# Performance work log

Measured on AMD Instinct MI355X. Metric: run time of the kernel, lower is better.

Reference implementation:

```python
import jax, jax.numpy as jnp
import numpy as np

# FP4 E2M1 representable magnitudes (sign handled separately)
_FP4_GRID = np.array([0.0, 0.5, 1.0, 1.5, 2.0, 3.0, 4.0, 6.0], dtype=np.float32)
_FP4_MIDS = (_FP4_GRID[:-1] + _FP4_GRID[1:]) / 2.0  # round-to-nearest boundaries


def fp4_quant_dequant(w):
    """Per-tensor absmax-scaled round-to-nearest FP4 (E2M1) fake quantization."""
    grid = jnp.asarray(_FP4_GRID, dtype=w.dtype)
    mids = jnp.asarray(_FP4_MIDS, dtype=w.dtype)
    scale = jnp.max(jnp.abs(w)) / 6.0  # map absmax -> top FP4 level
    a = jnp.abs(w) / scale
    idx = jnp.searchsorted(mids, a)  # nearest grid index via boundary search
    return grid[idx] * jnp.sign(w) * scale


def fp4_linear(x, W, b):
    # dequantized-weight matmul + bias, as in FP4Linear
    Wq = fp4_quant_dequant(W)
    return x @ Wq.T + b


def setup_inputs() -> dict:
    key = jax.random.key(0)
    k1, k2, k3, k4, k5 = jax.random.split(key, 5)
    B, D_IN, D_H, D_OUT = 8192, 2048, 8192, 2048
    x = jax.random.normal(k1, (B, D_IN), dtype=jnp.float32)
    W1 = jax.random.normal(k2, (D_H, D_IN), dtype=jnp.float32) * 0.02
    b1 = jax.random.normal(k3, (D_H,), dtype=jnp.float32) * 0.02
    W2 = jax.random.normal(k4, (D_OUT, D_H), dtype=jnp.float32) * 0.02
    b2 = jax.random.normal(k5, (D_OUT,), dtype=jnp.float32) * 0.02
    return {"x": x, "W1": W1, "b1": b1, "W2": W2, "b2": b2}


def reference(x, W1, b1, W2, b2):
    h = jax.nn.relu(fp4_linear(x, W1, b1))  # [B, hidden]
    y = fp4_linear(h, W2, b2)                # [B, out]
    return y
```

## Files before the change

kernel.cpp:

```cpp
#include <hip/hip_runtime.h>
#include <hip/hip_bf16.h>
#include <stdint.h>

typedef __attribute__((ext_vector_type(8))) short short8;
typedef __attribute__((ext_vector_type(4))) float f32x4;

#define AS1 __attribute__((address_space(1)))
#define AS3 __attribute__((address_space(3)))

static __device__ __forceinline__ unsigned short f2bf(float f) {
    unsigned int u = __float_as_uint(f);
    u += 0x7FFFu + ((u >> 16) & 1u);
    return (unsigned short)(u >> 16);
}

__global__ void init_amax(unsigned int* amax) {
    if (threadIdx.x < 2) amax[threadIdx.x] = 0u;
}

__global__ void absmax_kernel(const float4* __restrict__ w, size_t n4,
                              unsigned int* __restrict__ out) {
    float m = 0.0f;
    size_t i = (size_t)blockIdx.x * blockDim.x + threadIdx.x;
    size_t stride = (size_t)gridDim.x * blockDim.x;
    for (; i < n4; i += stride) {
        float4 v = w[i];
        m = fmaxf(m, fmaxf(fmaxf(fabsf(v.x), fabsf(v.y)),
                           fmaxf(fabsf(v.z), fabsf(v.w))));
    }
    #pragma unroll
    for (int off = 32; off > 0; off >>= 1)
        m = fmaxf(m, __shfl_down(m, off, 64));
    __shared__ float sm[4];
    int lane = threadIdx.x & 63, wid = threadIdx.x >> 6;
    if (lane == 0) sm[wid] = m;
    __syncthreads();
    if (threadIdx.x == 0) {
        float bm = fmaxf(fmaxf(sm[0], sm[1]), fmaxf(sm[2], sm[3]));
        atomicMax(out, __float_as_uint(bm));
    }
}

static __device__ __forceinline__ unsigned short quant_one(float wv, float scale) {
    float a = fabsf(wv) / scale;
    int idx = (a > 0.25f) + (a > 0.75f) + (a > 1.25f) + (a > 1.75f)
            + (a > 2.5f)  + (a > 3.5f)  + (a > 5.0f);
    const unsigned long long lo = 0x3FC03F803F000000ull;
    const unsigned long long hi = 0x40C0408040404000ull;
    unsigned long long tab = (idx < 4) ? lo : hi;
    unsigned short mag = (unsigned short)(tab >> ((idx & 3) * 16));
    unsigned short sgn = (unsigned short)((__float_as_uint(wv) >> 16) & 0x8000u);
    return (unsigned short)(mag | sgn);
}

__global__ void quant_kernel(const float4* __restrict__ w, size_t n4,
                             const unsigned int* __restrict__ amax,
                             ushort4* __restrict__ q) {
    const float scale = __uint_as_float(*amax) / 6.0f;
    size_t i = (size_t)blockIdx.x * blockDim.x + threadIdx.x;
    size_t stride = (size_t)gridDim.x * blockDim.x;
    for (; i < n4; i += stride) {
        float4 v = w[i];
        ushort4 o;
        o.x = quant_one(v.x, scale);
        o.y = quant_one(v.y, scale);
        o.z = quant_one(v.z, scale);
        o.w = quant_one(v.w, scale);
        q[i] = o;
    }
}

__global__ void cast_bf16_kernel(const float4* __restrict__ x, size_t n4,
                                 ushort4* __restrict__ o) {
    size_t i = (size_t)blockIdx.x * blockDim.x + threadIdx.x;
    size_t stride = (size_t)gridDim.x * blockDim.x;
    for (; i < n4; i += stride) {
        float4 v = x[i];
        ushort4 r;
        r.x = f2bf(v.x); r.y = f2bf(v.y); r.z = f2bf(v.z); r.w = f2bf(v.w);
        o[i] = r;
    }
}


#define STG(gp, ldsoff)                                                         \
    do {                                                                        \
        __builtin_amdgcn_global_load_lds((const AS1 unsigned int*)((gp) + goff0), \
            (AS3 unsigned int*)(lds + (ldsoff) + tid * 16), 16, 0, 0);          \
        __builtin_amdgcn_global_load_lds((const AS1 unsigned int*)((gp) + goff1), \
            (AS3 unsigned int*)(lds + (ldsoff) + 8192 + tid * 16), 16, 0, 0);   \
    } while (0)

#define LDB(base)                                                   \
    do {                                                            \
        _Pragma("unroll") for (int j = 0; j < 4; ++j) {             \
            b_[j][0] = *(const short8*)((base) + (j * 2 + 0) * 1024); \
            b_[j][1] = *(const short8*)((base) + (j * 2 + 1) * 1024); \
        }                                                           \
    } while (0)

#define LDA(base, off)                                                        \
    do {                                                                      \
        _Pragma("unroll") for (int i = 0; i < 4; ++i) {                       \
            a_[i][0] = *(const short8*)((base) + (off) + (i * 2 + 0) * 1024); \
            a_[i][1] = *(const short8*)((base) + (off) + (i * 2 + 1) * 1024); \
        }                                                                     \
    } while (0)

#define MQ1(I, J)                                                              \
    do {                                                                       \
        acc[I][J] = __builtin_amdgcn_mfma_f32_16x16x32_bf16(a_[(I) & 3][0],    \
                        b_[J][0], acc[I][J], 0, 0, 0);                         \
        acc[I][J] = __builtin_amdgcn_mfma_f32_16x16x32_bf16(a_[(I) & 3][1],    \
                        b_[J][1], acc[I][J], 0, 0, 0);                         \
    } while (0)

#define MFMA_Q(I0, J0)                                              \
    do {                                                            \
        MQ1((I0) + 0, (J0) + 0); MQ1((I0) + 1, (J0) + 0);           \
        MQ1((I0) + 2, (J0) + 0); MQ1((I0) + 3, (J0) + 0);           \
        MQ1((I0) + 0, (J0) + 1); MQ1((I0) + 1, (J0) + 1);           \
        MQ1((I0) + 2, (J0) + 1); MQ1((I0) + 3, (J0) + 1);           \
    } while (0)

#define BAR() __builtin_amdgcn_s_barrier()
#define PRIO(x) __builtin_amdgcn_s_setprio(x)

template <int RELU_BF16>
__global__ __launch_bounds__(512, 2)
void gemm8(const unsigned short* __restrict__ A,
           const unsigned short* __restrict__ B,
           const float* __restrict__ bias,
           const unsigned int* __restrict__ amax,
           float* __restrict__ outF,
           unsigned short* __restrict__ outH,
           int M, int N, int K, int gx) {
    __shared__ __align__(16) char lds[131072];

    const int tid  = threadIdx.x;
    const int lane = tid & 63;
    const int wid  = tid >> 6;
    const int wm   = wid >> 2;
    const int wn   = wid & 3;

    const int nwg = gridDim.x;
    const int wg  = blockIdx.x;
    const int swz = (wg & 7) * (nwg >> 3) + (wg >> 3);
    const int bx  = swz % gx;
    const int by  = swz / gx;
    const int col0 = bx * 256;
    const int row0 = by * 256;

    int sp = ((lane & 15) << 6) + ((lane >> 4) << 4);
    sp ^= ((sp >> 9) & 1) << 5;

    const char* ldsA_E = lds + wm * 16384 + sp;
    const char* ldsB_E = lds + 32768 + (wn >> 1) * 16384 + (wn & 1) * 8192 + sp;
    const char* ldsA_O = ldsA_E + 65536;
    const char* ldsB_O = ldsB_E + 65536;

    int goff0, goff1;
    {
        int o = tid * 16;
        int s = o >> 10, b = o & 1023;
        b ^= ((b >> 9) & 1) << 5;
        goff0 = (((s >> 1) << 4) + (b >> 6)) * K + ((s & 1) << 5) + ((b & 63) >> 1);
        o = 8192 + tid * 16;
        s = o >> 10; b = o & 1023;
        b ^= ((b >> 9) & 1) << 5;
        goff1 = (((s >> 1) << 4) + (b >> 6)) * K + ((s & 1) << 5) + ((b & 63) >> 1);
    }
    const unsigned short* pA0 = A + (size_t)row0 * K;
    const unsigned short* pA1 = A + (size_t)(row0 + 128) * K;
    const unsigned short* pB0 = B + (size_t)col0 * K;
    const unsigned short* pB1 = B + (size_t)(col0 + 128) * K;

    STG(pB0, 32768); STG(pB1, 49152); STG(pA0, 0); STG(pA1, 16384);
    STG(pB0 + 64, 98304); STG(pB1 + 64, 114688); STG(pA0 + 64, 65536);
    asm volatile("s_waitcnt vmcnt(6)");
    BAR();

    f32x4 acc[8][4] = {};
    short8 a_[4][2], b_[4][2];
    const int NIT = K >> 7;

    for (int it = 0; it < NIT; ++it) {
        const int o0 = it * 128;
        const bool more = it < NIT - 1;

        LDB(ldsB_E);
        LDA(ldsA_E, 0);
        STG(pA1 + o0 + 64, 81920);
        BAR();
        PRIO(1); MFMA_Q(0, 0); PRIO(0);
        BAR();
        if (more) STG(pB0 + o0 + 128, 32768);
        BAR();
        PRIO(1); MFMA_Q(0, 2); PRIO(0);
        BAR();
        LDA(ldsA_E, 8192);
        if (more) STG(pB1 + o0 + 128, 49152);
        BAR();
        PRIO(1); MFMA_Q(4, 2); PRIO(0);
        BAR();
        if (more) STG(pA0 + o0 + 128, 0);
        BAR();
        PRIO(1); MFMA_Q(4, 0); PRIO(0);
        if (more) { asm volatile("s_waitcnt vmcnt(6)"); }
        else      { asm volatile("s_waitcnt vmcnt(0)"); }
        BAR();
        LDB(ldsB_O);
        LDA(ldsA_O, 0);
        if (more) STG(pA1 + o0 + 128, 16384);
        BAR();
        PRIO(1); MFMA_Q(0, 0); PRIO(0);
        BAR();
        if (more) STG(pB0 + o0 + 192, 98304);
        BAR();
        PRIO(1); MFMA_Q(0, 2); PRIO(0);
        BAR();
        LDA(ldsA_O, 8192);
        if (more) STG(pB1 + o0 + 192, 114688);
        BAR();
        PRIO(1); MFMA_Q(4, 2); PRIO(0);
        BAR();
        if (more) STG(pA0 + o0 + 192, 65536);
        BAR();
        PRIO(1); MFMA_Q(4, 0); PRIO(0);
        asm volatile("s_waitcnt vmcnt(6)");
        BAR();
    }

    const float scale = __uint_as_float(*amax) / 6.0f;
    #pragma unroll
    for (int j = 0; j < 4; ++j) {
        const int col = col0 + wn * 64 + j * 16 + (lane & 15);
        const float bvv = bias[col];
        #pragma unroll
        for (int i = 0; i < 8; ++i) {
            const int rbase = row0 + wm * 128 + i * 16 + (lane >> 4) * 4;
            #pragma unroll
            for (int r = 0; r < 4; ++r) {
                float v = acc[i][j][r] * scale + bvv;
                if (RELU_BF16) {
                    v = fmaxf(v, 0.0f);
                    outH[(size_t)(rbase + r) * N + col] = f2bf(v);
                } else {
                    outF[(size_t)(rbase + r) * N + col] = v;
                }
            }
        }
    }
}

extern "C" void kernel_launch(void* const* d_in, const int* in_sizes, int n_in,
                              void* d_out, int out_size, void* d_ws, size_t ws_size,
                              hipStream_t stream) {
    const float* x  = (const float*)d_in[0];
    const float* W1 = (const float*)d_in[1];
    const float* b1 = (const float*)d_in[2];
    const float* W2 = (const float*)d_in[3];
    const float* b2 = (const float*)d_in[4];
    float* out = (float*)d_out;

    const int Bm = 8192, Din = 2048, Dh = 8192, Dout = 2048;
    const size_t nW1 = (size_t)Dh * Din;
    const size_t nW2 = (size_t)Dout * Dh;
    const size_t nX  = (size_t)Bm * Din;
    const size_t nH  = (size_t)Bm * Dh;

    const size_t need = 256 + 2 * (nW1 + nW2 + nX + nH);
    if (ws_size < need) return;

    uint8_t* ws = (uint8_t*)d_ws;
    unsigned int*   amax = (unsigned int*)ws;
    unsigned short* Q1 = (unsigned short*)(ws + 256);
    unsigned short* Q2 = Q1 + nW1;
    unsigned short* Xb = Q2 + nW2;
    unsigned short* H  = Xb + nX;

    init_amax<<<1, 64, 0, stream>>>(amax);
    absmax_kernel<<<1024, 256, 0, stream>>>((const float4*)W1, nW1 / 4, amax + 0);
    absmax_kernel<<<1024, 256, 0, stream>>>((const float4*)W2, nW2 / 4, amax + 1);
    quant_kernel<<<2048, 256, 0, stream>>>((const float4*)W1, nW1 / 4, amax + 0, (ushort4*)Q1);
    quant_kernel<<<2048, 256, 0, stream>>>((const float4*)W2, nW2 / 4, amax + 1, (ushort4*)Q2);
    cast_bf16_kernel<<<2048, 256, 0, stream>>>((const float4*)x, nX / 4, (ushort4*)Xb);

    gemm8<1><<<dim3((Dh / 256) * (Bm / 256)), 512, 0, stream>>>(
        Xb, Q1, b1, amax + 0, nullptr, H, Bm, Dh, Din, Dh / 256);
    gemm8<0><<<dim3((Dout / 256) * (Bm / 256)), 512, 0, stream>>>(
        H, Q2, b2, amax + 1, out, nullptr, Bm, Dout, Dh, Dout / 256);
}
```

Before: 582.9 us.

## Split B-fragment LDS loads across phases and peel last GEMM K-iteration

The main loop body becomes a macro, and the final K iteration is peeled so the steady-state loop carries no runtime 'more' checks. B fragments are now read from LDS in two halves, each just before the MFMA phase that uses it, with explicit lgkmcnt waits and sched_barriers. Two global-to-LDS stages are grouped into one phase, which removes one barrier pair per half-iteration. The aim is better overlap of LDS reads with MFMAs and fewer barriers, at the cost of fragile hand-placed waitcnt values that must match the number of outstanding LDS and VMEM ops.

```diff
diff --git a/kernel.cpp b/kernel.cpp
--- a/kernel.cpp
+++ b/kernel.cpp
@@ -91,12 +91,10 @@
             (AS3 unsigned int*)(lds + (ldsoff) + 8192 + tid * 16), 16, 0, 0);   \
     } while (0)
 
-#define LDB(base)                                                   \
-    do {                                                            \
-        _Pragma("unroll") for (int j = 0; j < 4; ++j) {             \
-            b_[j][0] = *(const short8*)((base) + (j * 2 + 0) * 1024); \
-            b_[j][1] = *(const short8*)((base) + (j * 2 + 1) * 1024); \
-        }                                                           \
+#define LDB2(base, J)                                                 \
+    do {                                                              \
+        b_[J][0] = *(const short8*)((base) + ((J) * 2 + 0) * 1024);   \
+        b_[J][1] = *(const short8*)((base) + ((J) * 2 + 1) * 1024);   \
     } while (0)
 
 #define LDA(base, off)                                                        \
@@ -125,6 +123,56 @@
 
 #define BAR() __builtin_amdgcn_s_barrier()
 #define PRIO(x) __builtin_amdgcn_s_setprio(x)
+
+#define PHASE(MF)                                   \
+    do {                                            \
+        BAR();                                      \
+        asm volatile("s_waitcnt lgkmcnt(0)");       \
+        __builtin_amdgcn_sched_barrier(0);          \
+        PRIO(1); MF; PRIO(0);                       \
+        BAR();                                      \
+    } while (0)
+
+#define KITER(MORE)                                                          \
+    do {                                                                     \
+                           \
+        LDB2(ldsB_E, 0); LDB2(ldsB_E, 1); LDA(ldsA_E, 0);                    \
+        STG(pA1 + o0 + 64, 81920);                                           \
+        asm volatile("s_waitcnt lgkmcnt(8)");                                \
+        PHASE(MFMA_Q(0, 0));                                                 \
+                                                         \
+        LDB2(ldsB_E, 2); LDB2(ldsB_E, 3);                                    \
+        PHASE(MFMA_Q(0, 2));                                                 \
+                                   \
+        LDA(ldsA_E, 8192);                                                   \
+        if (MORE) STG(pB0 + o0 + 128, 32768);                                \
+        PHASE(MFMA_Q(4, 2));                                                 \
+                            \
+        if (MORE) { STG(pB1 + o0 + 128, 49152); STG(pA0 + o0 + 128, 0); }    \
+        BAR();                                                               \
+        PRIO(1); MFMA_Q(4, 0); PRIO(0);                                      \
+        if (MORE) { asm volatile("s_waitcnt vmcnt(6)"); }                    \
+        else      { asm volatile("s_waitcnt vmcnt(0)"); }                    \
+        BAR();                                                               \
+                           \
+        LDB2(ldsB_O, 0); LDB2(ldsB_O, 1); LDA(ldsA_O, 0);                    \
+        if (MORE) STG(pA1 + o0 + 128, 16384);                                \
+        asm volatile("s_waitcnt lgkmcnt(8)");                                \
+        PHASE(MFMA_Q(0, 0));                                                 \
+                                                         \
+        LDB2(ldsB_O, 2); LDB2(ldsB_O, 3);                                    \
+        PHASE(MFMA_Q(0, 2));                                                 \
+                                   \
+        LDA(ldsA_O, 8192);                                                   \
+        if (MORE) STG(pB0 + o0 + 192, 98304);                                \
+        PHASE(MFMA_Q(4, 2));                                                 \
+                            \
+        if (MORE) { STG(pB1 + o0 + 192, 114688); STG(pA0 + o0 + 192, 65536); } \
+        BAR();                                                               \
+        PRIO(1); MFMA_Q(4, 0); PRIO(0);                                      \
+        if (MORE) { asm volatile("s_waitcnt vmcnt(6)"); }                    \
+        BAR();                                                               \
+    } while (0)
 
 template <int RELU_BF16>
 __global__ __launch_bounds__(512, 2)
@@ -184,51 +232,13 @@
     short8 a_[4][2], b_[4][2];
     const int NIT = K >> 7;
 
-    for (int it = 0; it < NIT; ++it) {
+    for (int it = 0; it < NIT - 1; ++it) {
         const int o0 = it * 128;
-        const bool more = it < NIT - 1;
-
-        LDB(ldsB_E);
-        LDA(ldsA_E, 0);
-        STG(pA1 + o0 + 64, 81920);
-        BAR();
-        PRIO(1); MFMA_Q(0, 0); PRIO(0);
-        BAR();
-        if (more) STG(pB0 + o0 + 128, 32768);
-        BAR();
-        PRIO(1); MFMA_Q(0, 2); PRIO(0);
-        BAR();
-        LDA(ldsA_E, 8192);
-        if (more) STG(pB1 + o0 + 128, 49152);
-        BAR();
-        PRIO(1); MFMA_Q(4, 2); PRIO(0);
-        BAR();
-        if (more) STG(pA0 + o0 + 128, 0);
-        BAR();
-        PRIO(1); MFMA_Q(4, 0); PRIO(0);
-        if (more) { asm volatile("s_waitcnt vmcnt(6)"); }
-        else      { asm volatile("s_waitcnt vmcnt(0)"); }
-        BAR();
-        LDB(ldsB_O);
-        LDA(ldsA_O, 0);
-        if (more) STG(pA1 + o0 + 128, 16384);
-        BAR();
-        PRIO(1); MFMA_Q(0, 0); PRIO(0);
-        BAR();
-        if (more) STG(pB0 + o0 + 192, 98304);
-        BAR();
-        PRIO(1); MFMA_Q(0, 2); PRIO(0);
-        BAR();
-        LDA(ldsA_O, 8192);
-        if (more) STG(pB1 + o0 + 192, 114688);
-        BAR();
-        PRIO(1); MFMA_Q(4, 2); PRIO(0);
-        BAR();
-        if (more) STG(pA0 + o0 + 192, 65536);
-        BAR();
-        PRIO(1); MFMA_Q(4, 0); PRIO(0);
-        asm volatile("s_waitcnt vmcnt(6)");
-        BAR();
+        KITER(1);
+    }
+    {
+        const int o0 = (NIT - 1) * 128;
+        KITER(0);
     }
 
     const float scale = __uint_as_float(*amax) / 6.0f;
```

New measurement: 584.3 us. No clear change (+0.2%).

## Restructure GEMM k-tile schedule with finer LDS fragment prefetch and fewer barriers

Applied to the files above, without the earlier changes.

Replaces the eight-phase per-half-tile schedule, which had many block barriers, with a KTILE macro. KTILE double-buffers A and B register fragments (aP/aQ, bE/bO) and uses explicit lgkmcnt waits so LDS reads overlap with MFMA groups. Global-to-LDS loads for the next tile are batched after a single barrier. The last iteration is peeled out so the loop body has no runtime `more` conditions. The aim is less barrier stall and better overlap of LDS reads with matrix math, at the cost of more live fragment registers and tighter manual waitcnt correctness.

```diff
diff --git a/kernel.cpp b/kernel.cpp
--- a/kernel.cpp
+++ b/kernel.cpp
@@ -83,48 +83,61 @@
 }
 
 
-#define STG(gp, ldsoff)                                                         \
-    do {                                                                        \
-        __builtin_amdgcn_global_load_lds((const AS1 unsigned int*)((gp) + goff0), \
-            (AS3 unsigned int*)(lds + (ldsoff) + tid * 16), 16, 0, 0);          \
-        __builtin_amdgcn_global_load_lds((const AS1 unsigned int*)((gp) + goff1), \
-            (AS3 unsigned int*)(lds + (ldsoff) + 8192 + tid * 16), 16, 0, 0);   \
-    } while (0)
-
-#define LDB(base)                                                   \
-    do {                                                            \
-        _Pragma("unroll") for (int j = 0; j < 4; ++j) {             \
-            b_[j][0] = *(const short8*)((base) + (j * 2 + 0) * 1024); \
-            b_[j][1] = *(const short8*)((base) + (j * 2 + 1) * 1024); \
-        }                                                           \
-    } while (0)
-
-#define LDA(base, off)                                                        \
+#define GLL(gp, dst)                                                    \
+    __builtin_amdgcn_global_load_lds((const AS1 unsigned int*)(gp),     \
+        (AS3 unsigned int*)(dst), 16, 0, 0)
+
+#define STG(gp, ldsoff)                                       \
+    do {                                                      \
+        GLL((gp) + goff0, lds + (ldsoff) + tid * 16);         \
+        GLL((gp) + goff1, lds + (ldsoff) + 8192 + tid * 16);  \
+    } while (0)
+
+#define LD4(dst, base, s0)                                                    \
     do {                                                                      \
-        _Pragma("unroll") for (int i = 0; i < 4; ++i) {                       \
-            a_[i][0] = *(const short8*)((base) + (off) + (i * 2 + 0) * 1024); \
-            a_[i][1] = *(const short8*)((base) + (off) + (i * 2 + 1) * 1024); \
-        }                                                                     \
-    } while (0)
-
-#define MQ1(I, J)                                                              \
+        _Pragma("unroll") for (int _i = 0; _i < 4; ++_i)                      \
+            dst[_i] = *(const short8*)((base) + ((s0) + _i * 2) * 1024);      \
+    } while (0)
+
+#define MFG(AH, ARR, BRR)                                                      \
     do {                                                                       \
-        acc[I][J] = __builtin_amdgcn_mfma_f32_16x16x32_bf16(a_[(I) & 3][0],    \
-                        b_[J][0], acc[I][J], 0, 0, 0);                         \
-        acc[I][J] = __builtin_amdgcn_mfma_f32_16x16x32_bf16(a_[(I) & 3][1],    \
-                        b_[J][1], acc[I][J], 0, 0, 0);                         \
-    } while (0)
-
-#define MFMA_Q(I0, J0)                                              \
-    do {                                                            \
-        MQ1((I0) + 0, (J0) + 0); MQ1((I0) + 1, (J0) + 0);           \
-        MQ1((I0) + 2, (J0) + 0); MQ1((I0) + 3, (J0) + 0);           \
-        MQ1((I0) + 0, (J0) + 1); MQ1((I0) + 1, (J0) + 1);           \
-        MQ1((I0) + 2, (J0) + 1); MQ1((I0) + 3, (J0) + 1);           \
-    } while (0)
-
-#define BAR() __builtin_amdgcn_s_barrier()
+        _Pragma("unroll") for (int _i = 0; _i < 4; ++_i)                       \
+            _Pragma("unroll") for (int _j = 0; _j < 4; ++_j)                   \
+                acc[(AH) * 4 + _i][_j] =                                       \
+                    __builtin_amdgcn_mfma_f32_16x16x32_bf16(                   \
+                        ARR[_i], BRR[_j], acc[(AH) * 4 + _i][_j], 0, 0, 0);    \
+    } while (0)
+
+#define BAR()  __builtin_amdgcn_s_barrier()
 #define PRIO(x) __builtin_amdgcn_s_setprio(x)
+#define SCHB() __builtin_amdgcn_sched_barrier(0)
+#define LGKM(n) do { SCHB(); asm volatile("s_waitcnt lgkmcnt(" #n ")"); SCHB(); } while (0)
+
+#define KTILE(ldsB_, ldsA_, MA1, kA1, oA1, MORE, kNXT, oB0, oB1, oA0, VMODE)   \
+    do {                                                                       \
+        LD4(bE, ldsB_, 0);                                  \
+        LD4(aP, ldsA_, 0);                                     \
+        LD4(aQ, ldsA_, 8);                                     \
+        if (MA1) STG(pA1 + (kA1), oA1);                                        \
+        LGKM(4);                                \
+        PRIO(1); MFG(0, aP, bE); PRIO(0);                                      \
+        LD4(bO, ldsB_, 1);                                        \
+        LD4(aP, ldsA_, 1);                                     \
+        LGKM(8);                               \
+        PRIO(1); MFG(1, aQ, bE); PRIO(0);                                      \
+        LD4(aQ, ldsA_, 9);                                     \
+        LGKM(4);                              \
+        PRIO(1); MFG(0, aP, bO); PRIO(0);                                      \
+        LGKM(0);                            \
+        BAR();                                                                 \
+        if (MORE) { STG(pB0 + (kNXT), oB0); STG(pB1 + (kNXT), oB1);            \
+                    STG(pA0 + (kNXT), oA0); }                                  \
+        SCHB();                                                                \
+        PRIO(1); MFG(1, aQ, bO); PRIO(0);                                      \
+        if (VMODE == 2) { asm volatile("s_waitcnt vmcnt(6)"); }                \
+        if (VMODE == 1) { asm volatile("s_waitcnt vmcnt(0)"); }                \
+        BAR();                                                                 \
+    } while (0)
 
 template <int RELU_BF16>
 __global__ __launch_bounds__(512, 2)
@@ -181,54 +194,22 @@
     BAR();
 
     f32x4 acc[8][4] = {};
-    short8 a_[4][2], b_[4][2];
+    short8 aP[4], aQ[4], bE[4], bO[4];
     const int NIT = K >> 7;
 
-    for (int it = 0; it < NIT; ++it) {
+    for (int it = 0; it < NIT - 1; ++it) {
         const int o0 = it * 128;
-        const bool more = it < NIT - 1;
-
-        LDB(ldsB_E);
-        LDA(ldsA_E, 0);
-        STG(pA1 + o0 + 64, 81920);
-        BAR();
-        PRIO(1); MFMA_Q(0, 0); PRIO(0);
-        BAR();
-        if (more) STG(pB0 + o0 + 128, 32768);
-        BAR();
-        PRIO(1); MFMA_Q(0, 2); PRIO(0);
-        BAR();
-        LDA(ldsA_E, 8192);
-        if (more) STG(pB1 + o0 + 128, 49152);
-        BAR();
-        PRIO(1); MFMA_Q(4, 2); PRIO(0);
-        BAR();
-        if (more) STG(pA0 + o0 + 128, 0);
-        BAR();
-        PRIO(1); MFMA_Q(4, 0); PRIO(0);
-        if (more) { asm volatile("s_waitcnt vmcnt(6)"); }
-        else      { asm volatile("s_waitcnt vmcnt(0)"); }
-        BAR();
-        LDB(ldsB_O);
-        LDA(ldsA_O, 0);
-        if (more) STG(pA1 + o0 + 128, 16384);
-        BAR();
-        PRIO(1); MFMA_Q(0, 0); PRIO(0);
-        BAR();
-        if (more) STG(pB0 + o0 + 192, 98304);
-        BAR();
-        PRIO(1); MFMA_Q(0, 2); PRIO(0);
-        BAR();
-        LDA(ldsA_O, 8192);
-        if (more) STG(pB1 + o0 + 192, 114688);
-        BAR();
-        PRIO(1); MFMA_Q(4, 2); PRIO(0);
-        BAR();
-        if (more) STG(pA0 + o0 + 192, 65536);
-        BAR();
-        PRIO(1); MFMA_Q(4, 0); PRIO(0);
-        asm volatile("s_waitcnt vmcnt(6)");
-        BAR();
+        KTILE(ldsB_E, ldsA_E, 1, o0 + 64, 81920,
+              1, o0 + 128, 32768, 49152, 0, 2);
+        KTILE(ldsB_O, ldsA_O, 1, o0 + 128, 16384,
+              1, o0 + 192, 98304, 114688, 65536, 2);
+    }
+    {
+        const int o0 = (NIT - 1) * 128;
+        KTILE(ldsB_E, ldsA_E, 1, o0 + 64, 81920,
+              0, 0, 0, 0, 0, 1);
+        KTILE(ldsB_O, ldsA_O, 0, 0, 0,
+              0, 0, 0, 0, 0, 0);
     }
 
     const float scale = __uint_as_float(*amax) / 6.0f;
```

Measured after the change: 569.1 us. 1.02x faster.
